# Kernel optimization log

Hardware: AMD Instinct MI355X
Metric: run time of the kernel (lower is better)

## Reference

```python
import jax, jax.numpy as jnp
import numpy as np

D_MODEL = 2048
N_HEADS = 8
EXPAND_K = 1
EXPAND_V = 2
DK = D_MODEL * EXPAND_K // N_HEADS      # 256 per-head key dim
DV = D_MODEL * EXPAND_V // N_HEADS      # 512 per-head value dim
INTER = 5632
EPS = 1e-6
CHUNK = 64


def setup_inputs() -> dict:
    key = jax.random.key(0)
    ks = jax.random.split(key, 12)
    d = D_MODEL
    s = lambda fan_in: 1.0 / np.sqrt(fan_in)
    return {
        "hidden_states": jax.random.normal(ks[0], (2, 2048, d), jnp.float32),
        "attn_norm_w": jnp.ones((d,), jnp.float32),
        "q_w": jax.random.normal(ks[1], (d, d * EXPAND_K), jnp.float32) * s(d),
        "k_w": jax.random.normal(ks[2], (d, d * EXPAND_K), jnp.float32) * s(d),
        "v_w": jax.random.normal(ks[3], (d, d * EXPAND_V), jnp.float32) * s(d),
        "g_w": jax.random.normal(ks[4], (d, d * EXPAND_V), jnp.float32) * s(d),
        "o_w": jax.random.normal(ks[5], (d * EXPAND_V, d), jnp.float32) * s(d * EXPAND_V),
        "gnorm_w": jnp.ones((DV,), jnp.float32),
        "mlp_norm_w": jnp.ones((d,), jnp.float32),
        "gate_w": jax.random.normal(ks[6], (d, INTER * 2), jnp.float32) * s(d),
        "down_w": jax.random.normal(ks[7], (INTER, d), jnp.float32) * s(INTER),
    }


def rmsnorm(x, w, eps=EPS):
    return x * jax.lax.rsqrt(jnp.mean(x * x, axis=-1, keepdims=True) + eps) * w


def rope(x):
    # x: [B, T, H, D]; non-interleaved rotary on full head dim
    T, D = x.shape[1], x.shape[-1]
    inv_freq = 1.0 / (10000.0 ** (jnp.arange(0, D, 2, dtype=jnp.float32) / D))
    ang = jnp.arange(T, dtype=jnp.float32)[:, None] * inv_freq  # [T, D/2]
    cos = jnp.cos(ang)[None, :, None, :]
    sin = jnp.sin(ang)[None, :, None, :]
    x1, x2 = jnp.split(x, 2, axis=-1)
    return jnp.concatenate([x1 * cos - x2 * sin, x2 * cos + x1 * sin], axis=-1)


def chunk_retention(q, k, v):
    # q,k: [B,T,H,Dk], v: [B,T,H,Dv]; chunkwise-recurrent RetNet retention
    B, T, H, Dk = q.shape
    Dv = v.shape[-1]
    C = CHUNK
    N = T // C
    gamma = 1.0 - jnp.exp2(-5.0 - jnp.arange(H, dtype=jnp.float32))  # [H]
    i = jnp.arange(C, dtype=jnp.float32)
    diff = i[:, None] - i[None, :]
    Dmask = jnp.where(diff >= 0, gamma[:, None, None] ** diff, 0.0)   # [H,C,C]
    cross_decay = gamma[:, None] ** (i[None, :] + 1.0)                # [H,C]
    k_decay = gamma[:, None] ** (C - 1.0 - i[None, :])                # [H,C]
    chunk_decay = gamma ** C                                          # [H]

    # -> [N, B, H, C, D]
    to_chunks = lambda x: jnp.moveaxis(
        x.reshape(B, N, C, H, x.shape[-1]).transpose(0, 1, 3, 2, 4), 1, 0)
    qc, kc, vc = to_chunks(q), to_chunks(k), to_chunks(v)

    def body(S, inp):
        qb, kb, vb = inp  # [B,H,C,Dk/Dv]
        attn = jnp.einsum('bhid,bhjd->bhij', qb, kb) * Dmask
        o_intra = jnp.einsum('bhij,bhje->bhie', attn, vb)
        o_cross = jnp.einsum('bhid,bhde->bhie', qb * cross_decay[None, :, :, None], S)
        S = chunk_decay[None, :, None, None] * S + \
            jnp.einsum('bhid,bhie->bhde', kb * k_decay[None, :, :, None], vb)
        return S, o_intra + o_cross

    S0 = jnp.zeros((B, H, Dk, Dv), q.dtype)
    _, o = jax.lax.scan(body, S0, (qc, kc, vc))  # o: [N,B,H,C,Dv]
    return jnp.moveaxis(o, 0, 1).transpose(0, 1, 3, 2, 4).reshape(B, T, H, Dv)


def reference(hidden_states, attn_norm_w, q_w, k_w, v_w, g_w, o_w, gnorm_w,
              mlp_norm_w, gate_w, down_w):
    B, T, d = hidden_states.shape
    residual = hidden_states
    h = rmsnorm(hidden_states, attn_norm_w)

    # MultiScaleRetention
    q = (h @ q_w).reshape(B, T, N_HEADS, DK)
    k = (h @ k_w).reshape(B, T, N_HEADS, DK)
    v = (h @ v_w).reshape(B, T, N_HEADS, DV)
    g = (h @ g_w).reshape(B, T, N_HEADS, DV)
    q, k = rope(q), rope(k)
    q = q * (DK ** -0.5)
    o = chunk_retention(q, k, v)
    # fused RMSNorm + swish gate (per head over Dv)
    o = rmsnorm(o, gnorm_w) * (g * jax.nn.sigmoid(g))
    h = o.reshape(B, T, N_HEADS * DV) @ o_w

    # fused-residual RMSNorm
    residual = h + residual
    h = rmsnorm(residual, mlp_norm_w)

    # SwiGLU MLP
    y = h @ gate_w
    gate, y = jnp.split(y, 2, axis=-1)
    h = (gate * jax.nn.sigmoid(gate) * y) @ down_w
    return residual + h
```

## Files before the change

### kernel.cpp

```cpp
#include <hip/hip_runtime.h>
#include <cstdint>
#include <cstddef>

typedef unsigned short u16;
typedef __attribute__((ext_vector_type(4))) float f32x4;
typedef __attribute__((ext_vector_type(4))) unsigned int u32x4;

__device__ __forceinline__ float b2f(u16 u) {
  union { unsigned int i; float f; } x; x.i = ((unsigned int)u) << 16; return x.f;
}
__device__ __forceinline__ u16 f2b(float f) {
  union { float f; unsigned int i; } x; x.f = f;
  unsigned int i = x.i;
  i += 0x7fffu + ((i >> 16) & 1u);
  return (u16)(i >> 16);
}

__device__ __forceinline__ void mfma_bf16(f32x4& c, u32x4 a, u32x4 b) {
  asm("v_mfma_f32_16x16x32_bf16 %0, %1, %2, %0" : "+v"(c) : "v"(a), "v"(b));
}

__device__ __forceinline__ void async_ld16(const u16* g, u16* l) {
  typedef __attribute__((address_space(1))) const unsigned int GU;
  typedef __attribute__((address_space(3))) unsigned int LU;
  __builtin_amdgcn_global_load_lds((GU*)g, (LU*)l, 16, 0, 0);
}

__global__ __launch_bounds__(256)
void transpose_cast_kernel(const float* __restrict__ in, u16* __restrict__ out,
                           int K, int N, int ldin) {
  __shared__ float tile[64][65];
  const int nb = N >> 6;
  const int bk = blockIdx.x / nb, bn = blockIdx.x % nb;
  const int k0 = bk * 64, n0 = bn * 64;
  const int tid = threadIdx.x;
#pragma unroll
  for (int p = 0; p < 16; ++p) {
    int idx = p * 256 + tid;
    int r = idx >> 6, c = idx & 63;
    tile[r][c] = in[(size_t)(k0 + r) * ldin + n0 + c];
  }
  __syncthreads();
#pragma unroll
  for (int p = 0; p < 16; ++p) {
    int idx = p * 256 + tid;
    int r = idx >> 6, c = idx & 63;
    out[(size_t)(n0 + r) * K + k0 + c] = f2b(tile[c][r]);
  }
}

__global__ __launch_bounds__(256)
void transpose_k_kernel(const u16* __restrict__ qk, u16* __restrict__ kt) {
  __shared__ u16 tile[64][72];
  const int bid = blockIdx.x;
  const int dd = bid & 3, tt = (bid >> 2) & 31;
  const int h = (bid >> 7) & 7, b = bid >> 10;
  const int t0 = tt * 64, d0 = dd * 64;
  const int tid = threadIdx.x;
#pragma unroll
  for (int p = 0; p < 2; ++p) {
    int idx = p * 256 + tid;
    int r = idx >> 3, cq = (idx & 7) * 8;
    *(uint4*)&tile[r][cq] =
        *(const uint4*)&qk[(size_t)(b * 2048 + t0 + r) * 4096 + 2048 + h * 256 + d0 + cq];
  }
  __syncthreads();
#pragma unroll
  for (int p = 0; p < 2; ++p) {
    int idx = p * 256 + tid;
    int r = idx >> 3, cq = (idx & 7) * 8;
    union { u16 h8[8]; uint4 v4; } o;
#pragma unroll
    for (int j = 0; j < 8; ++j) o.h8[j] = tile[cq + j][r];
    *(uint4*)&kt[((size_t)(b * 8 + h) * 256 + d0 + r) * 2048 + t0 + cq] = o.v4;
  }
}

__global__ __launch_bounds__(256)
void rmsnorm_cast_kernel(const float* __restrict__ x, const float* __restrict__ w,
                         u16* __restrict__ out) {
  const int row = blockIdx.x, tid = threadIdx.x;
  const float* xr = x + (size_t)row * 2048;
  float4 a = ((const float4*)xr)[tid * 2];
  float4 b = ((const float4*)xr)[tid * 2 + 1];
  float ss = a.x*a.x + a.y*a.y + a.z*a.z + a.w*a.w
           + b.x*b.x + b.y*b.y + b.z*b.z + b.w*b.w;
#pragma unroll
  for (int m = 32; m; m >>= 1) ss += __shfl_xor(ss, m);
  __shared__ float ps[4];
  if ((tid & 63) == 0) ps[tid >> 6] = ss;
  __syncthreads();
  const float sc = rsqrtf((ps[0] + ps[1] + ps[2] + ps[3]) * (1.0f / 2048.0f) + 1e-6f);
  const int base = tid * 8;
  const float vals[8] = {a.x, a.y, a.z, a.w, b.x, b.y, b.z, b.w};
  union { u16 h[8]; uint4 v4[2]; } o;
#pragma unroll
  for (int j = 0; j < 8; ++j) o.h[j] = f2b(vals[j] * sc * w[base + j]);
  *(uint4*)&out[(size_t)row * 2048 + base] = o.v4[0];
  *(uint4*)&out[(size_t)row * 2048 + base + 8] = o.v4[1];
}

__global__ __launch_bounds__(256)
void rmsnorm_bf16_kernel(const u16* __restrict__ x, const float* __restrict__ w,
                         u16* __restrict__ out) {
  const int row = blockIdx.x, tid = threadIdx.x;
  union { uint4 v4; u16 h[8]; } p;
  p.v4 = *(const uint4*)&x[(size_t)row * 2048 + tid * 8];
  float v[8];
  float ss = 0.f;
#pragma unroll
  for (int j = 0; j < 8; ++j) { v[j] = b2f(p.h[j]); ss += v[j] * v[j]; }
#pragma unroll
  for (int m = 32; m; m >>= 1) ss += __shfl_xor(ss, m);
  __shared__ float ps[4];
  if ((tid & 63) == 0) ps[tid >> 6] = ss;
  __syncthreads();
  const float sc = rsqrtf((ps[0] + ps[1] + ps[2] + ps[3]) * (1.0f / 2048.0f) + 1e-6f);
  union { u16 h[8]; uint4 v4; } o;
#pragma unroll
  for (int j = 0; j < 8; ++j) o.h[j] = f2b(v[j] * sc * w[tid * 8 + j]);
  *(uint4*)&out[(size_t)row * 2048 + tid * 8] = o.v4;
}

__global__ __launch_bounds__(256)
void rope_table_kernel(float* __restrict__ ct, float* __restrict__ st) {
  const int idx = blockIdx.x * 256 + threadIdx.x;
  const int t = idx >> 7, i = idx & 127;
  const float e = -(float)i * (0.0078125f * log2f(10000.0f));
  const float ang = (float)t * exp2f(e);
  ct[idx] = cosf(ang);
  st[idx] = sinf(ang);
}

__global__ __launch_bounds__(256)
void rope_apply_kernel(u16* __restrict__ x, const float* __restrict__ ct,
                       const float* __restrict__ st, int qoff, float scale) {
  const int gid = blockIdx.x * 256 + threadIdx.x;
  const int r = gid >> 8;
  const int rem = gid & 255;
  const int h = rem >> 5;
  const int i4 = (rem & 31) * 4;
  const int t = r & 2047;
  const size_t o1 = (size_t)r * 4096 + qoff + h * 256 + i4;
  union { ushort4 v; u16 h4[4]; } p1, p2, q1, q2;
  p1.v = *(ushort4*)&x[o1];
  p2.v = *(ushort4*)&x[o1 + 128];
  const float4 c = *(const float4*)&ct[t * 128 + i4];
  const float4 s = *(const float4*)&st[t * 128 + i4];
  const float cc[4] = {c.x, c.y, c.z, c.w};
  const float sn[4] = {s.x, s.y, s.z, s.w};
#pragma unroll
  for (int j = 0; j < 4; ++j) {
    float x1 = b2f(p1.h4[j]), x2 = b2f(p2.h4[j]);
    q1.h4[j] = f2b((x1 * cc[j] - x2 * sn[j]) * scale);
    q2.h4[j] = f2b((x2 * cc[j] + x1 * sn[j]) * scale);
  }
  *(ushort4*)&x[o1] = q1.v;
  *(ushort4*)&x[o1 + 128] = q2.v;
}

template <int BM, int EPI>
__global__ __launch_bounds__(512, 2)
void gemm3(const u16* __restrict__ A, const u16* __restrict__ Bt,
           void* Cout, const float* fsrc, const u16* hsrc,
           int N, int K, int lda, int pm, int pn, int gw) {
  constexpr int MF = BM / 32;
  constexpr int AS16 = BM * 4;
  constexpr int SLOT16 = AS16 + 1024;
  constexpr int LA = BM / 128;
  constexpr int VMC = 2 * (LA + 2);
  __shared__ __align__(16) u16 lds[4 * SLOT16 * 8];

  const int tid = threadIdx.x;
  const int l = tid & 63, w = tid >> 6;
  const int lr = l & 15, hi = l >> 4;
  const int wm = w >> 2, wn = w & 3;
  const int xcd = blockIdx.x & 7;
  const int j = blockIdx.x >> 3;
  const int gx = xcd % gw, gy = xcd / gw;
  const int bm = gx * pm + j / pn;
  const int bn = gy * pn + j % pn;
  const int nt = K >> 5;

  const u16* Ap[LA]; const u16* Bp[2];
#pragma unroll
  for (int t = 0; t < LA; ++t) {
    int s = t * 512 + tid;
    int row = s >> 2, chL = (s & 3) ^ ((s >> 3) & 3);
    Ap[t] = A + (size_t)(bm * BM + row) * lda + chL * 8;
  }
#pragma unroll
  for (int t = 0; t < 2; ++t) {
    int s = t * 512 + tid;
    int row = s >> 2, chL = (s & 3) ^ ((s >> 3) & 3);
    Bp[t] = Bt + (size_t)(bn * 256 + row) * K + chL * 8;
  }
  int aoff[MF], boff[4];
#pragma unroll
  for (int mf = 0; mf < MF; ++mf) {
    int r = wm * (BM / 2) + mf * 16 + lr;
    aoff[mf] = r * 4 + (hi ^ ((r >> 1) & 3));
  }
#pragma unroll
  for (int nf = 0; nf < 4; ++nf) {
    int r = wn * 64 + nf * 16 + lr;
    boff[nf] = AS16 + r * 4 + (hi ^ ((r >> 1) & 3));
  }

  f32x4 acc[MF][4];
#pragma unroll
  for (int m = 0; m < MF; ++m)
#pragma unroll
    for (int n = 0; n < 4; ++n) acc[m][n] = (f32x4){0.f, 0.f, 0.f, 0.f};

#pragma unroll
  for (int tt = 0; tt < 3; ++tt) {
    const int sb = tt * SLOT16;
#pragma unroll
    for (int t = 0; t < LA; ++t)
      async_ld16(Ap[t] + tt * 32, &lds[(size_t)(sb + t * 512 + w * 64) * 8]);
#pragma unroll
    for (int t = 0; t < 2; ++t)
      async_ld16(Bp[t] + tt * 32, &lds[(size_t)(sb + AS16 + t * 512 + w * 64) * 8]);
    __builtin_amdgcn_sched_barrier(0);
  }
  asm volatile("s_waitcnt vmcnt(%0)" :: "n"(VMC) : "memory");
  __builtin_amdgcn_sched_barrier(0);
  __builtin_amdgcn_s_barrier();
  __builtin_amdgcn_sched_barrier(0);

  for (int i = 0; i < nt; ++i) {
    int pf = i + 3; if (pf >= nt) pf -= nt;
    const int sc = (i & 3) * SLOT16;
    const int sp = ((i + 3) & 3) * SLOT16;
    u32x4 bf[4], af[4];
#pragma unroll
    for (int nf = 0; nf < 4; ++nf) bf[nf] = *(const u32x4*)&lds[(size_t)(sc + boff[nf]) * 8];
#pragma unroll
    for (int mf = 0; mf < 4; ++mf) af[mf] = *(const u32x4*)&lds[(size_t)(sc + aoff[mf]) * 8];
#pragma unroll
    for (int t = 0; t < LA; ++t)
      async_ld16(Ap[t] + pf * 32, &lds[(size_t)(sp + t * 512 + w * 64) * 8]);
    if (MF == 4) {
#pragma unroll
      for (int t = 0; t < 2; ++t)
        async_ld16(Bp[t] + pf * 32, &lds[(size_t)(sp + AS16 + t * 512 + w * 64) * 8]);
    }
    __builtin_amdgcn_sched_barrier(0);
    __builtin_amdgcn_s_barrier();
    __builtin_amdgcn_s_setprio(1);
#pragma unroll
    for (int mf = 0; mf < 4; ++mf)
#pragma unroll
      for (int nf = 0; nf < 4; ++nf) mfma_bf16(acc[mf][nf], af[mf], bf[nf]);
    __builtin_amdgcn_s_setprio(0);
    __builtin_amdgcn_sched_barrier(0);
    if (MF == 8) {
      __builtin_amdgcn_s_barrier();
#pragma unroll
      for (int mf = 0; mf < 4; ++mf)
        af[mf] = *(const u32x4*)&lds[(size_t)(sc + aoff[4 + mf]) * 8];
#pragma unroll
      for (int t = 0; t < 2; ++t)
        async_ld16(Bp[t] + pf * 32, &lds[(size_t)(sp + AS16 + t * 512 + w * 64) * 8]);
      __builtin_amdgcn_sched_barrier(0);
      __builtin_amdgcn_s_barrier();
      __builtin_amdgcn_s_setprio(1);
#pragma unroll
      for (int mf = 0; mf < 4; ++mf)
#pragma unroll
        for (int nf = 0; nf < 4; ++nf) mfma_bf16(acc[4 + mf][nf], af[mf], bf[nf]);
      __builtin_amdgcn_s_setprio(0);
      __builtin_amdgcn_sched_barrier(0);
    }
    asm volatile("s_waitcnt vmcnt(%0)" :: "n"(VMC) : "memory");
    __builtin_amdgcn_sched_barrier(0);
    __builtin_amdgcn_s_barrier();
    __builtin_amdgcn_sched_barrier(0);
  }

  const size_t crow0 = (size_t)(bm * BM + wm * (BM / 2));
  const int ccol0 = bn * 256 + wn * 64;
#pragma unroll
  for (int m = 0; m < MF; ++m)
#pragma unroll
    for (int n = 0; n < 4; ++n)
#pragma unroll
      for (int j2 = 0; j2 < 4; ++j2) {
        size_t r = crow0 + m * 16 + hi * 4 + j2;
        size_t c = (size_t)(ccol0 + n * 16 + lr);
        size_t idx = r * N + c;
        float a = acc[m][n][j2];
        if (EPI == 1) {
          ((u16*)Cout)[idx] = f2b(a);
        } else if (EPI == 2) {
          ((float*)Cout)[idx] = a + b2f(hsrc[idx]);
        } else if (EPI == 3) {
          float u = b2f(hsrc[idx]);
          ((u16*)Cout)[idx] = f2b(a / (1.0f + expf(-a)) * u);
        } else {
          ((u16*)Cout)[idx] = f2b(a + fsrc[idx]);
        }
      }
}

#define LGK 264
#define LGC 72
__global__ __launch_bounds__(512)
void retention_kernel(const u16* __restrict__ qk, const u16* __restrict__ kt,
                      const u16* __restrict__ v, u16* __restrict__ o) {
  __shared__ __align__(16) u16 ks[64 * LGK];
  __shared__ __align__(16) u16 stb[32 * LGK];
  __shared__ __align__(16) u16 ktd[256 * LGC];
  __shared__ __align__(16) u16 vts[32 * LGC];
  __shared__ __align__(16) u16 ab[64 * LGC];
  __shared__ float kdt[64];

  const int tid = threadIdx.x;
  const int l = tid & 63, w = tid >> 6;
  const int lr = l & 15, hi = l >> 4;
  const int wr = w >> 1;
  const int eb = w & 1;
  const int bid = blockIdx.x;
  const int g = bid & 15;
  const int sl = bid >> 4;
  const int hh = g & 7;
  const int b = g >> 3;
  const float gamma = 1.0f - exp2f(-5.0f - (float)hh);
  const float lg = log2f(gamma);
  const float cdk = exp2f(64.0f * lg);
  const int e0 = sl * 32;

  if (tid < 64) kdt[tid] = exp2f((float)(63 - tid) * lg);
  __syncthreads();

  f32x4 st[4];
#pragma unroll
  for (int t = 0; t < 4; ++t) st[t] = (f32x4){0.f, 0.f, 0.f, 0.f};

  for (int n = 0; n < 32; ++n) {
    const int row0 = b * 2048 + n * 64;
    const int t0 = n * 64;
#pragma unroll
    for (int t = 0; t < 4; ++t)
#pragma unroll
      for (int j = 0; j < 4; ++j)
        stb[(eb * 16 + hi * 4 + j) * LGK + (wr * 4 + t) * 16 + lr] = f2b(st[t][j]);
    u32x4 qf[8];
#pragma unroll
    for (int kk = 0; kk < 8; ++kk)
      qf[kk] = *(const u32x4*)&qk[(size_t)(row0 + wr * 16 + lr) * 4096 +
                                  hh * 256 + kk * 32 + hi * 8];
#pragma unroll
    for (int p = 0; p < 4; ++p) {
      int idx = p * 512 + tid;
      int c = idx >> 5, s = (idx & 31) * 8;
      *(uint4*)&ks[c * LGK + s] =
          *(const uint4*)&qk[(size_t)(row0 + c) * 4096 + 2048 + hh * 256 + s];
    }
#pragma unroll
    for (int p = 0; p < 4; ++p) {
      int idx = p * 512 + tid;
      int d = idx >> 3, cq = (idx & 7) * 8;
      union { uint4 v4; u16 h[8]; } pk;
      pk.v4 = *(const uint4*)&kt[((size_t)(b * 8 + hh) * 256 + d) * 2048 + t0 + cq];
      union { u16 h[8]; uint4 v4; } wo;
#pragma unroll
      for (int j2 = 0; j2 < 8; ++j2)
        wo.h[j2] = f2b(b2f(pk.h[j2]) * kdt[cq + j2]);
      *(uint4*)&ktd[d * LGC + cq] = wo.v4;
    }
#pragma unroll
    for (int p = 0; p < 4; ++p) {
      int c = (tid >> 5) + p * 16, e = tid & 31;
      vts[e * LGC + c] = v[(size_t)(row0 + c) * 4096 + hh * 512 + e0 + e];
    }
    __syncthreads();

    f32x4 att[2];
    att[0] = (f32x4){0.f, 0.f, 0.f, 0.f};
    att[1] = (f32x4){0.f, 0.f, 0.f, 0.f};
#pragma unroll
    for (int kk = 0; kk < 8; ++kk) {
#pragma unroll
      for (int jf = 0; jf < 2; ++jf) {
        u32x4 bb = *(const u32x4*)&ks[(eb * 32 + jf * 16 + lr) * LGK + kk * 32 + hi * 8];
        mfma_bf16(att[jf], qf[kk], bb);
      }
    }
#pragma unroll
    for (int jf = 0; jf < 2; ++jf)
#pragma unroll
      for (int j = 0; j < 4; ++j) {
        int i = wr * 16 + hi * 4 + j;
        int jc = eb * 32 + jf * 16 + lr;
        float mv = (i >= jc) ? exp2f((float)(i - jc) * lg) : 0.0f;
        ab[i * LGC + jc] = f2b(att[jf][j] * mv);
      }
    f32x4 occ = (f32x4){0.f, 0.f, 0.f, 0.f};
#pragma unroll
    for (int kk = 0; kk < 8; ++kk) {
      u32x4 bb = *(const u32x4*)&stb[(eb * 16 + lr) * LGK + kk * 32 + hi * 8];
      mfma_bf16(occ, qf[kk], bb);
    }
    __syncthreads();

#pragma unroll
    for (int j = 0; j < 4; ++j) {
      int i = wr * 16 + hi * 4 + j;
      occ[j] *= exp2f((float)(i + 1) * lg);
    }
#pragma unroll
    for (int kk = 0; kk < 2; ++kk) {
      u32x4 aa = *(const u32x4*)&ab[(wr * 16 + lr) * LGC + kk * 32 + hi * 8];
      u32x4 bb = *(const u32x4*)&vts[(eb * 16 + lr) * LGC + kk * 32 + hi * 8];
      mfma_bf16(occ, aa, bb);
    }
#pragma unroll
    for (int j = 0; j < 4; ++j) {
      int i = wr * 16 + hi * 4 + j;
      o[(size_t)(row0 + i) * 4096 + hh * 512 + e0 + eb * 16 + lr] = f2b(occ[j]);
    }
#pragma unroll
    for (int t = 0; t < 4; ++t) {
      st[t][0] *= cdk; st[t][1] *= cdk; st[t][2] *= cdk; st[t][3] *= cdk;
    }
#pragma unroll
    for (int kk = 0; kk < 2; ++kk) {
      u32x4 aa = *(const u32x4*)&vts[(eb * 16 + lr) * LGC + kk * 32 + hi * 8];
#pragma unroll
      for (int t = 0; t < 4; ++t) {
        u32x4 bb = *(const u32x4*)&ktd[((wr * 4 + t) * 16 + lr) * LGC + kk * 32 + hi * 8];
        mfma_bf16(st[t], aa, bb);
      }
    }
    __syncthreads();
  }
}

__global__ __launch_bounds__(64)
void gating_kernel(u16* __restrict__ o, const u16* __restrict__ g,
                   const float* __restrict__ gnw) {
  const int blk = blockIdx.x;
  const size_t base = (size_t)blk * 512;
  const int l = threadIdx.x;
  union { uint4 v4; u16 h[8]; } ov, gv;
  ov.v4 = *(const uint4*)&o[base + l * 8];
  float x[8];
  float ss = 0.f;
#pragma unroll
  for (int j = 0; j < 8; ++j) { x[j] = b2f(ov.h[j]); ss += x[j] * x[j]; }
#pragma unroll
  for (int m = 32; m; m >>= 1) ss += __shfl_xor(ss, m);
  const float sc = rsqrtf(ss * (1.0f / 512.0f) + 1e-6f);
  gv.v4 = *(const uint4*)&g[base + l * 8];
  union { u16 h[8]; uint4 v4; } ou;
#pragma unroll
  for (int j = 0; j < 8; ++j) {
    float gvf = b2f(gv.h[j]);
    float sig = 1.0f / (1.0f + expf(-gvf));
    ou.h[j] = f2b(x[j] * sc * gnw[l * 8 + j] * gvf * sig);
  }
  *(uint4*)&o[base + l * 8] = ou.v4;
}

extern "C" void kernel_launch(void* const* d_in, const int* in_sizes, int n_in,
                              void* d_out, int out_size, void* d_ws, size_t ws_size,
                              hipStream_t stream) {
  (void)in_sizes; (void)n_in; (void)out_size; (void)ws_size;
  const float* hidden      = (const float*)d_in[0];
  const float* attn_norm_w = (const float*)d_in[1];
  const float* q_w         = (const float*)d_in[2];
  const float* k_w         = (const float*)d_in[3];
  const float* v_w         = (const float*)d_in[4];
  const float* g_w         = (const float*)d_in[5];
  const float* o_w         = (const float*)d_in[6];
  const float* gnorm_w     = (const float*)d_in[7];
  const float* mlp_norm_w  = (const float*)d_in[8];
  const float* gate_w      = (const float*)d_in[9];
  const float* down_w      = (const float*)d_in[10];
  float* outp = (float*)d_out;

  char* ws = (char*)d_ws;
  size_t off = 0;
  auto alloc = [&](size_t bytes) -> char* {
    char* p = ws + off;
    off += (bytes + 255) & ~(size_t)255;
    return p;
  };
  u16*   W    = (u16*)alloc(23068672ULL);
  float* ctab = (float*)alloc(1048576ULL);
  float* stab = (float*)alloc(1048576ULL);
  u16*   hb   = (u16*)alloc(16777216ULL);
  u16*   qkb  = (u16*)alloc(33554432ULL);
  u16*   vb   = (u16*)alloc(33554432ULL);
  u16*   gb   = (u16*)alloc(33554432ULL);
  u16*   ob   = (u16*)alloc(33554432ULL);
  u16*   resb = (u16*)alloc(16777216ULL);
  u16*   ybU  = qkb;
  u16*   kt   = W;

  rope_table_kernel<<<1024, 256, 0, stream>>>(ctab, stab);
  rmsnorm_cast_kernel<<<4096, 256, 0, stream>>>(hidden, attn_norm_w, hb);

  transpose_cast_kernel<<<1024, 256, 0, stream>>>(q_w, W, 2048, 2048, 2048);
  transpose_cast_kernel<<<1024, 256, 0, stream>>>(k_w, W + 2048ULL * 2048, 2048, 2048, 2048);
  gemm3<256, 1><<<256, 512, 0, stream>>>(hb, W, (void*)qkb, nullptr, nullptr,
                                         4096, 2048, 2048, 8, 4, 2);
  transpose_cast_kernel<<<2048, 256, 0, stream>>>(v_w, W, 2048, 4096, 4096);
  gemm3<256, 1><<<256, 512, 0, stream>>>(hb, W, (void*)vb, nullptr, nullptr,
                                         4096, 2048, 2048, 8, 4, 2);
  transpose_cast_kernel<<<2048, 256, 0, stream>>>(g_w, W, 2048, 4096, 4096);
  gemm3<256, 1><<<256, 512, 0, stream>>>(hb, W, (void*)gb, nullptr, nullptr,
                                         4096, 2048, 2048, 8, 4, 2);

  rope_apply_kernel<<<4096, 256, 0, stream>>>(qkb, ctab, stab, 0, 0.0625f);
  rope_apply_kernel<<<4096, 256, 0, stream>>>(qkb, ctab, stab, 2048, 1.0f);
  transpose_k_kernel<<<2048, 256, 0, stream>>>(qkb, kt);

  retention_kernel<<<256, 512, 0, stream>>>(qkb, kt, vb, ob);

  gating_kernel<<<32768, 64, 0, stream>>>(ob, gb, gnorm_w);

  transpose_cast_kernel<<<2048, 256, 0, stream>>>(o_w, W, 4096, 2048, 2048);
  gemm3<128, 4><<<256, 512, 0, stream>>>(ob, W, (void*)resb, hidden, nullptr,
                                         2048, 4096, 4096, 8, 4, 4);

  rmsnorm_bf16_kernel<<<4096, 256, 0, stream>>>(resb, mlp_norm_w, hb);

  transpose_cast_kernel<<<2816, 256, 0, stream>>>(gate_w + 5632, W, 2048, 5632, 11264);
  gemm3<256, 1><<<352, 512, 0, stream>>>(hb, W, (void*)ybU, nullptr, nullptr,
                                         5632, 2048, 2048, 4, 11, 4);
  transpose_cast_kernel<<<2816, 256, 0, stream>>>(gate_w, W, 2048, 5632, 11264);
  gemm3<256, 3><<<352, 512, 0, stream>>>(hb, W, (void*)ybU, nullptr, ybU,
                                         5632, 2048, 2048, 4, 11, 4);

  transpose_cast_kernel<<<2816, 256, 0, stream>>>(down_w, W, 5632, 2048, 2048);
  gemm3<128, 2><<<256, 512, 0, stream>>>(ybU, W, (void*)outp, nullptr, resb,
                                         2048, 5632, 5632, 8, 4, 4);
}
```

Measured before the change: 963.5 us.

## Rewrite GEMM mainloop as double-buffered 64-wide K tiles with split prefetch

Replaces the 4-slot, 32-wide-K ring buffer in the GEMM with two buffers of 64-wide K tiles, each split into two 32-wide halves. Global-to-LDS loads for the next halves are interleaved between MFMA phases. This halves the number of loop iterations and the full barrier/wait points per K element, and should hide load latency better. The o_proj and down_proj launches also get a different XCD block-grouping (pm/pn/gw), which changes L2 reuse. The cost is a more intricate barrier schedule and vmcnt accounting that have to stay correct.

```diff
diff --git a/kernel.cpp b/kernel.cpp
--- a/kernel.cpp
+++ b/kernel.cpp
@@ -161,50 +161,44 @@
 
 template <int BM, int EPI>
 __global__ __launch_bounds__(512, 2)
-void gemm3(const u16* __restrict__ A, const u16* __restrict__ Bt,
+void gemm4(const u16* __restrict__ A, const u16* __restrict__ Bt,
            void* Cout, const float* fsrc, const u16* hsrc,
            int N, int K, int lda, int pm, int pn, int gw) {
   constexpr int MF = BM / 32;
-  constexpr int AS16 = BM * 4;
-  constexpr int SLOT16 = AS16 + 1024;
   constexpr int LA = BM / 128;
-  constexpr int VMC = 2 * (LA + 2);
-  __shared__ __align__(16) u16 lds[4 * SLOT16 * 8];
+  constexpr int AH = BM * 64;
+  constexpr int BH = 16384;
+  constexpr int BUFB = 2 * AH + 2 * BH;
+  constexpr int VMC = (BM == 256) ? 8 : 6;
+  __shared__ __align__(16) char smem[2 * BUFB];
 
   const int tid = threadIdx.x;
   const int l = tid & 63, w = tid >> 6;
   const int lr = l & 15, hi = l >> 4;
   const int wm = w >> 2, wn = w & 3;
   const int xcd = blockIdx.x & 7;
-  const int j = blockIdx.x >> 3;
+  const int jj = blockIdx.x >> 3;
   const int gx = xcd % gw, gy = xcd / gw;
-  const int bm = gx * pm + j / pn;
-  const int bn = gy * pn + j % pn;
-  const int nt = K >> 5;
-
-  const u16* Ap[LA]; const u16* Bp[2];
-#pragma unroll
-  for (int t = 0; t < LA; ++t) {
-    int s = t * 512 + tid;
-    int row = s >> 2, chL = (s & 3) ^ ((s >> 3) & 3);
-    Ap[t] = A + (size_t)(bm * BM + row) * lda + chL * 8;
-  }
-#pragma unroll
-  for (int t = 0; t < 2; ++t) {
-    int s = t * 512 + tid;
-    int row = s >> 2, chL = (s & 3) ^ ((s >> 3) & 3);
-    Bp[t] = Bt + (size_t)(bn * 256 + row) * K + chL * 8;
-  }
+  const int bm = gx * pm + jj / pn;
+  const int bn = gy * pn + jj % pn;
+  const int nt = K >> 6;
+
+  const int rA = tid >> 2;
+  const int chx = (tid & 3) ^ ((tid >> 3) & 3);
+  const u16* Ag = A + (size_t)(bm * BM + rA) * lda + chx * 8;
+  const u16* Bg = Bt + (size_t)(bn * 256 + rA) * K + chx * 8;
+  const int wb = w * 1024;
+
   int aoff[MF], boff[4];
 #pragma unroll
   for (int mf = 0; mf < MF; ++mf) {
     int r = wm * (BM / 2) + mf * 16 + lr;
-    aoff[mf] = r * 4 + (hi ^ ((r >> 1) & 3));
+    aoff[mf] = (r * 4 + (hi ^ ((r >> 1) & 3))) * 16;
   }
 #pragma unroll
   for (int nf = 0; nf < 4; ++nf) {
     int r = wn * 64 + nf * 16 + lr;
-    boff[nf] = AS16 + r * 4 + (hi ^ ((r >> 1) & 3));
+    boff[nf] = (r * 4 + (hi ^ ((r >> 1) & 3))) * 16;
   }
 
   f32x4 acc[MF][4];
@@ -212,72 +206,80 @@
   for (int m = 0; m < MF; ++m)
 #pragma unroll
     for (int n = 0; n < 4; ++n) acc[m][n] = (f32x4){0.f, 0.f, 0.f, 0.f};
-
-#pragma unroll
-  for (int tt = 0; tt < 3; ++tt) {
-    const int sb = tt * SLOT16;
-#pragma unroll
-    for (int t = 0; t < LA; ++t)
-      async_ld16(Ap[t] + tt * 32, &lds[(size_t)(sb + t * 512 + w * 64) * 8]);
-#pragma unroll
-    for (int t = 0; t < 2; ++t)
-      async_ld16(Bp[t] + tt * 32, &lds[(size_t)(sb + AS16 + t * 512 + w * 64) * 8]);
-    __builtin_amdgcn_sched_barrier(0);
-  }
-  asm volatile("s_waitcnt vmcnt(%0)" :: "n"(VMC) : "memory");
-  __builtin_amdgcn_sched_barrier(0);
-  __builtin_amdgcn_s_barrier();
-  __builtin_amdgcn_sched_barrier(0);
+  u32x4 af[4], bf[4];
+
+#define STA(kt, ks, bb)                                                        \
+  { _Pragma("unroll") for (int t = 0; t < LA; ++t)                             \
+      async_ld16(Ag + (size_t)t * 128 * lda + (kt) * 64 + (ks) * 32,           \
+                 (u16*)(smem + (bb) * BUFB + (ks) * AH + t * 8192 + wb)); }
+#define STB(kt, ks, bb)                                                        \
+  { _Pragma("unroll") for (int t = 0; t < 2; ++t)                              \
+      async_ld16(Bg + (size_t)t * 128 * K + (kt) * 64 + (ks) * 32,             \
+                 (u16*)(smem + (bb) * BUFB + 2 * AH + (ks) * BH + t * 8192 + wb)); }
+#define RDA(mh, ks, bb)                                                        \
+  { _Pragma("unroll") for (int mf = 0; mf < 4; ++mf)                           \
+      af[mf] = *(const u32x4*)(smem + (bb) * BUFB + (ks) * AH + aoff[(mh) * 4 + mf]); }
+#define RDB(ks, bb)                                                            \
+  { _Pragma("unroll") for (int nf = 0; nf < 4; ++nf)                           \
+      bf[nf] = *(const u32x4*)(smem + (bb) * BUFB + 2 * AH + (ks) * BH + boff[nf]); }
+#define MM(mh)                                                                 \
+  { _Pragma("unroll") for (int mf = 0; mf < 4; ++mf)                           \
+      _Pragma("unroll") for (int nf = 0; nf < 4; ++nf)                         \
+        mfma_bf16(acc[(mh) * 4 + mf][nf], af[mf], bf[nf]); }
+#define SB   __builtin_amdgcn_sched_barrier(0)
+#define BARR __builtin_amdgcn_s_barrier()
+#define VMW  asm volatile("s_waitcnt vmcnt(%0)" :: "n"(VMC) : "memory")
+
+  STA(0, 0, 0); STB(0, 0, 0); STA(0, 1, 0); STB(0, 1, 0);
+  STA(1, 0, 1); STB(1, 0, 1);
+  SB; VMW; SB; BARR; SB;
 
   for (int i = 0; i < nt; ++i) {
-    int pf = i + 3; if (pf >= nt) pf -= nt;
-    const int sc = (i & 3) * SLOT16;
-    const int sp = ((i + 3) & 3) * SLOT16;
-    u32x4 bf[4], af[4];
-#pragma unroll
-    for (int nf = 0; nf < 4; ++nf) bf[nf] = *(const u32x4*)&lds[(size_t)(sc + boff[nf]) * 8];
-#pragma unroll
-    for (int mf = 0; mf < 4; ++mf) af[mf] = *(const u32x4*)&lds[(size_t)(sc + aoff[mf]) * 8];
-#pragma unroll
-    for (int t = 0; t < LA; ++t)
-      async_ld16(Ap[t] + pf * 32, &lds[(size_t)(sp + t * 512 + w * 64) * 8]);
-    if (MF == 4) {
-#pragma unroll
-      for (int t = 0; t < 2; ++t)
-        async_ld16(Bp[t] + pf * 32, &lds[(size_t)(sp + AS16 + t * 512 + w * 64) * 8]);
-    }
-    __builtin_amdgcn_sched_barrier(0);
-    __builtin_amdgcn_s_barrier();
-    __builtin_amdgcn_s_setprio(1);
-#pragma unroll
-    for (int mf = 0; mf < 4; ++mf)
-#pragma unroll
-      for (int nf = 0; nf < 4; ++nf) mfma_bf16(acc[mf][nf], af[mf], bf[nf]);
-    __builtin_amdgcn_s_setprio(0);
-    __builtin_amdgcn_sched_barrier(0);
-    if (MF == 8) {
-      __builtin_amdgcn_s_barrier();
-#pragma unroll
-      for (int mf = 0; mf < 4; ++mf)
-        af[mf] = *(const u32x4*)&lds[(size_t)(sc + aoff[4 + mf]) * 8];
-#pragma unroll
-      for (int t = 0; t < 2; ++t)
-        async_ld16(Bp[t] + pf * 32, &lds[(size_t)(sp + AS16 + t * 512 + w * 64) * 8]);
-      __builtin_amdgcn_sched_barrier(0);
-      __builtin_amdgcn_s_barrier();
-      __builtin_amdgcn_s_setprio(1);
-#pragma unroll
-      for (int mf = 0; mf < 4; ++mf)
-#pragma unroll
-        for (int nf = 0; nf < 4; ++nf) mfma_bf16(acc[4 + mf][nf], af[mf], bf[nf]);
-      __builtin_amdgcn_s_setprio(0);
-      __builtin_amdgcn_sched_barrier(0);
-    }
-    asm volatile("s_waitcnt vmcnt(%0)" :: "n"(VMC) : "memory");
-    __builtin_amdgcn_sched_barrier(0);
-    __builtin_amdgcn_s_barrier();
-    __builtin_amdgcn_sched_barrier(0);
-  }
+    const int bb = i & 1, ob = bb ^ 1;
+    const int t1 = (i + 1 < nt) ? i + 1 : 0;
+    const int t2 = (i + 2 < nt) ? i + 2 : 0;
+    if (BM == 256) {
+      RDA(0, 0, bb); RDB(0, bb);
+      STA(t1, 1, ob);
+      SB; BARR;
+      __builtin_amdgcn_s_setprio(1); MM(0); __builtin_amdgcn_s_setprio(0);
+      SB; BARR; SB;
+      RDA(1, 0, bb);
+      STB(t1, 1, ob);
+      SB; BARR;
+      __builtin_amdgcn_s_setprio(1); MM(1); __builtin_amdgcn_s_setprio(0);
+      SB; VMW; BARR; SB;
+      RDA(0, 1, bb); RDB(1, bb);
+      STA(t2, 0, bb);
+      SB; BARR;
+      __builtin_amdgcn_s_setprio(1); MM(0); __builtin_amdgcn_s_setprio(0);
+      SB; BARR; SB;
+      RDA(1, 1, bb);
+      STB(t2, 0, bb);
+      SB; BARR;
+      __builtin_amdgcn_s_setprio(1); MM(1); __builtin_amdgcn_s_setprio(0);
+      SB; VMW; BARR; SB;
+    } else {
+      RDA(0, 0, bb); RDB(0, bb);
+      STA(t1, 1, ob); STB(t1, 1, ob);
+      SB; BARR;
+      __builtin_amdgcn_s_setprio(1); MM(0); __builtin_amdgcn_s_setprio(0);
+      SB; VMW; BARR; SB;
+      RDA(0, 1, bb); RDB(1, bb);
+      STA(t2, 0, bb); STB(t2, 0, bb);
+      SB; BARR;
+      __builtin_amdgcn_s_setprio(1); MM(0); __builtin_amdgcn_s_setprio(0);
+      SB; VMW; BARR; SB;
+    }
+  }
+#undef STA
+#undef STB
+#undef RDA
+#undef RDB
+#undef MM
+#undef SB
+#undef BARR
+#undef VMW
 
   const size_t crow0 = (size_t)(bm * BM + wm * (BM / 2));
   const int ccol0 = bn * 256 + wn * 64;
@@ -505,13 +507,13 @@
 
   transpose_cast_kernel<<<1024, 256, 0, stream>>>(q_w, W, 2048, 2048, 2048);
   transpose_cast_kernel<<<1024, 256, 0, stream>>>(k_w, W + 2048ULL * 2048, 2048, 2048, 2048);
-  gemm3<256, 1><<<256, 512, 0, stream>>>(hb, W, (void*)qkb, nullptr, nullptr,
+  gemm4<256, 1><<<256, 512, 0, stream>>>(hb, W, (void*)qkb, nullptr, nullptr,
                                          4096, 2048, 2048, 8, 4, 2);
   transpose_cast_kernel<<<2048, 256, 0, stream>>>(v_w, W, 2048, 4096, 4096);
-  gemm3<256, 1><<<256, 512, 0, stream>>>(hb, W, (void*)vb, nullptr, nullptr,
+  gemm4<256, 1><<<256, 512, 0, stream>>>(hb, W, (void*)vb, nullptr, nullptr,
                                          4096, 2048, 2048, 8, 4, 2);
   transpose_cast_kernel<<<2048, 256, 0, stream>>>(g_w, W, 2048, 4096, 4096);
-  gemm3<256, 1><<<256, 512, 0, stream>>>(hb, W, (void*)gb, nullptr, nullptr,
+  gemm4<256, 1><<<256, 512, 0, stream>>>(hb, W, (void*)gb, nullptr, nullptr,
                                          4096, 2048, 2048, 8, 4, 2);
 
   rope_apply_kernel<<<4096, 256, 0, stream>>>(qkb, ctab, stab, 0, 0.0625f);
@@ -523,19 +525,19 @@
   gating_kernel<<<32768, 64, 0, stream>>>(ob, gb, gnorm_w);
 
   transpose_cast_kernel<<<2048, 256, 0, stream>>>(o_w, W, 4096, 2048, 2048);
-  gemm3<128, 4><<<256, 512, 0, stream>>>(ob, W, (void*)resb, hidden, nullptr,
-                                         2048, 4096, 4096, 8, 4, 4);
+  gemm4<128, 4><<<256, 512, 0, stream>>>(ob, W, (void*)resb, hidden, nullptr,
+                                         2048, 4096, 4096, 16, 2, 2);
 
   rmsnorm_bf16_kernel<<<4096, 256, 0, stream>>>(resb, mlp_norm_w, hb);
 
   transpose_cast_kernel<<<2816, 256, 0, stream>>>(gate_w + 5632, W, 2048, 5632, 11264);
-  gemm3<256, 1><<<352, 512, 0, stream>>>(hb, W, (void*)ybU, nullptr, nullptr,
+  gemm4<256, 1><<<352, 512, 0, stream>>>(hb, W, (void*)ybU, nullptr, nullptr,
                                          5632, 2048, 2048, 4, 11, 4);
   transpose_cast_kernel<<<2816, 256, 0, stream>>>(gate_w, W, 2048, 5632, 11264);
-  gemm3<256, 3><<<352, 512, 0, stream>>>(hb, W, (void*)ybU, nullptr, ybU,
+  gemm4<256, 3><<<352, 512, 0, stream>>>(hb, W, (void*)ybU, nullptr, ybU,
                                          5632, 2048, 2048, 4, 11, 4);
 
   transpose_cast_kernel<<<2816, 256, 0, stream>>>(down_w, W, 5632, 2048, 2048);
-  gemm3<128, 2><<<256, 512, 0, stream>>>(ybU, W, (void*)outp, nullptr, resb,
-                                         2048, 5632, 5632, 8, 4, 4);
-}
+  gemm4<128, 2><<<256, 512, 0, stream>>>(ybU, W, (void*)outp, nullptr, resb,
+                                         2048, 5632, 5632, 16, 2, 2);
+}
```

New measurement: 935.8 us. 2.9% less time.
